# Performance work log

Hardware: AMD Instinct MI355X
Metric: run time of the kernel (lower is better)

Reference implementation:

```python
import jax, jax.numpy as jnp
import numpy as np


def _conv1x1(x, w, b=None):
    # x: [B,C,H,W], w: [O,C]
    y = jnp.einsum('bchw,oc->bohw', x, w)
    if b is not None:
        y = y + b[None, :, None, None]
    return y


def _conv3x3_dilated(x, w, b, dil):
    p = dil  # padding == dilation keeps spatial size for 3x3 kernels
    y = jax.lax.conv_general_dilated(
        x, w, window_strides=(1, 1), padding=((p, p), (p, p)),
        rhs_dilation=(dil, dil), dimension_numbers=('NCHW', 'OIHW', 'NCHW'))
    return y + b[None, :, None, None]


def _upsample2x_align_corners(x):
    # bilinear, align_corners=True, scale factor 2
    B, C, H, W = x.shape
    oh, ow = 2 * H, 2 * W
    ys = jnp.linspace(0.0, H - 1.0, oh)
    xs = jnp.linspace(0.0, W - 1.0, ow)
    y0 = jnp.floor(ys).astype(jnp.int32)
    x0 = jnp.floor(xs).astype(jnp.int32)
    y1 = jnp.minimum(y0 + 1, H - 1)
    x1 = jnp.minimum(x0 + 1, W - 1)
    wy = (ys - y0)[None, None, :, None]
    wx = (xs - x0)[None, None, None, :]
    gt = x[:, :, y0, :]
    gb = x[:, :, y1, :]
    top = gt[:, :, :, x0] * (1 - wx) + gt[:, :, :, x1] * wx
    bot = gb[:, :, :, x0] * (1 - wx) + gb[:, :, :, x1] * wx
    return top * (1 - wy) + bot * wy


def _gr(ftr, ck_w, ck_b, avg_w, max_w, gcn_w):
    # GR module: attention-diagonal graph conv with degree normalization
    B, C, H, W = ftr.shape
    HW = H * W
    # ChannelAttention_diag -> diagonal entries cw: [B, M]
    avg = ftr.mean(axis=(2, 3))
    mx = ftr.max(axis=(2, 3))
    cw = jax.nn.sigmoid(jax.nn.relu(avg @ avg_w.T) + jax.nn.relu(mx @ max_w.T))  # [B,M]
    k = jax.nn.relu(_conv1x1(ftr, ck_w, ck_b)).reshape(B, -1, HW)  # [B,M,HW]
    q = jnp.swapaxes(k, 1, 2)  # [B,HW,M]
    # A = sigmoid(q @ diag(cw) @ k); degree d = rowsum(A)^(-1/2)
    A = jax.nn.sigmoid(jnp.einsum('bim,bm,bmj->bij', q, cw, k))  # [B,HW,HW]
    d = A.sum(axis=2) ** -0.5  # [B,HW]
    P = d[:, :, None] * q  # D^{-1/2} @ q, [B,HW,M]
    X = jnp.swapaxes(ftr.reshape(B, C, HW), 1, 2)  # [B,HW,C]
    PtX = jnp.einsum('bjm,bjc->bmc', P, X)  # [B,M,C]
    LX = X - jnp.einsum('bim,bmc->bic', P, cw[:, :, None] * PtX)
    Y = X + LX @ gcn_w  # GCN (no bias)
    return jnp.swapaxes(Y, 1, 2).reshape(B, C, H, W)


def setup_inputs() -> dict:
    key = jax.random.key(0)
    ks = jax.random.split(key, 20)
    B, C = 64, 1024
    Cq = C // 4  # 256
    Mi = Cq // 2  # 128, ChannelAttention inter channels
    s = 0.02
    inp = {
        'x_cur': jax.random.normal(ks[0], (B, C, 16, 16), jnp.float32),
        'x_lat': jax.random.normal(ks[1], (B, C, 8, 8), jnp.float32),
        'conv_w': jax.random.normal(ks[2], (Cq, C), jnp.float32) * s,
        'conv_b': jax.random.normal(ks[3], (Cq,), jnp.float32) * s,
        'conv1_w': jax.random.normal(ks[4], (C, Cq), jnp.float32) * s,
        'conv1_b': jax.random.normal(ks[5], (C,), jnp.float32) * s,
        'conv3_w': jax.random.normal(ks[6], (C, 3 * Cq), jnp.float32) * s,
        'conv3_b': jax.random.normal(ks[7], (C,), jnp.float32) * s,
        'rate0_w': jax.random.normal(ks[8], (Cq, C, 3, 3), jnp.float32) * s,
        'rate0_b': jax.random.normal(ks[9], (Cq,), jnp.float32) * s,
        'rate1_w': jax.random.normal(ks[10], (Cq, C, 3, 3), jnp.float32) * s,
        'rate1_b': jax.random.normal(ks[11], (Cq,), jnp.float32) * s,
        'rate2_w': jax.random.normal(ks[12], (Cq, C, 3, 3), jnp.float32) * s,
        'rate2_b': jax.random.normal(ks[13], (Cq,), jnp.float32) * s,
        'gr_ck_w': jax.random.normal(ks[14], (Mi, Cq), jnp.float32) * s,
        'gr_ck_b': jax.random.normal(ks[15], (Mi,), jnp.float32) * s,
        'gr_avg_w': jax.random.normal(ks[16], (Mi, Cq), jnp.float32) * s,
        'gr_max_w': jax.random.normal(ks[17], (Mi, Cq), jnp.float32) * s,
        'gr_gcn_w': jax.random.normal(ks[18], (Cq, Cq), jnp.float32) * s,
        'pre': 1,
    }
    return inp


def reference(x_cur, x_lat, conv_w, conv_b, conv1_w, conv1_b, conv3_w, conv3_b,
              rate0_w, rate0_b, rate1_w, rate1_b, rate2_w, rate2_b,
              gr_ck_w, gr_ck_b, gr_avg_w, gr_max_w, gr_gcn_w, pre):
    # pre == 1 path of Graph_aspp.forward
    gr_args = (gr_ck_w, gr_ck_b, gr_avg_w, gr_max_w, gr_gcn_w)
    x_sum = x_cur * _upsample2x_align_corners(x_lat) + x_cur
    f1 = _conv3x3_dilated(x_sum, rate0_w, rate0_b, 1) + _conv1x1(x_sum, conv_w, conv_b)
    x1 = _gr(f1, *gr_args)
    feature = _conv1x1(f1, conv1_w, conv1_b) + x_sum
    f2 = _conv3x3_dilated(feature, rate1_w, rate1_b, 2) + _conv1x1(feature, conv_w, conv_b)
    x2 = _gr(f2, *gr_args)
    feature = _conv1x1(f2, conv1_w, conv1_b) + x_sum
    f3 = _conv3x3_dilated(feature, rate2_w, rate2_b, 4) + _conv1x1(feature, conv_w, conv_b)
    x3 = _gr(f3, *gr_args)
    cat = jnp.concatenate((x1, x2, x3), axis=1)
    return _conv1x1(cat, conv3_w, conv3_b)
```

## Files before the change

kernel.cpp:

```cpp
#include <hip/hip_runtime.h>

typedef unsigned short ushort_t;
typedef unsigned int uint32;
typedef __attribute__((ext_vector_type(8))) unsigned short ushort8;
typedef __attribute__((ext_vector_type(8))) __bf16 bf16x8;
typedef __attribute__((ext_vector_type(4))) float f32x4;

__device__ __forceinline__ ushort_t f2b(float f) {
    union { float f; uint32 u; } v; v.f = f;
    uint32 r = v.u + 0x7fffu + ((v.u >> 16) & 1u);
    return (ushort_t)(r >> 16);
}
__device__ __forceinline__ float b2f(ushort_t b) {
    union { uint32 u; float f; } v; v.u = ((uint32)b) << 16;
    return v.f;
}
__device__ __forceinline__ float sigm(float x) { return 1.f / (1.f + __expf(-x)); }

__device__ __forceinline__ void gload_lds16(const void* g, void* l) {
    __builtin_amdgcn_global_load_lds(
        (__attribute__((address_space(1))) void*)g,
        (__attribute__((address_space(3))) void*)l, 16, 0, 0);
}

constexpr int EPI_RELU  = 1;
constexpr int EPI_FQ    = 2;
constexpr int EPI_SIG   = 3;
constexpr int EPI_XG    = 4;
constexpr int EPI_NEGCW = 5;
constexpr int EPI_Y     = 6;
constexpr int EPI_OUTT  = 7;

struct GemmP {
    const ushort_t* A; const ushort_t* B;
    const ushort_t* A2; const ushort_t* B2;
    long long aBatch, bBatch, a2Batch, b2Batch;
    int lda, ldb, lda2, ldb2;
    int Ksub, kSplit, dil;
    const float* bias;
    const ushort_t* res; long long resBatch; int ldres;
    ushort_t* obf; long long oBatch; int ldo;
    ushort_t* obf2;
    float* of32;
    const float* cw;
    const float* rscale;
    float* dsum;
    const ushort_t* zpage;
};

__device__ __forceinline__ void big_body(ushort_t* aT, ushort_t* bT,
                                         const GemmP& p, int bx, int by, int z) {
    const int tid = threadIdx.x;
    const int m0 = bx * 128, n0 = by * 128;
    const int lane = tid & 63, wid = tid >> 6;
    const int l15 = lane & 15, l16 = lane >> 4;
    const int wr = wid >> 1, wc = wid & 1;
    const int lrow = lane >> 3;
    const int sgran = (lane & 7) ^ lrow;

    int ayy[4], axx[4];
    const ushort_t* aBase[4];
    const ushort_t* bBase[4];
#pragma unroll
    for (int i = 0; i < 4; ++i) {
        int row = wid * 32 + i * 8 + lrow;
        int m = m0 + row;
        int bb = m >> 8;
        ayy[i] = (m >> 4) & 15; axx[i] = m & 15;
        aBase[i] = p.A + (long long)bb * 262144 + sgran * 8;
        bBase[i] = p.B + (long long)(n0 + row) * p.ldb + sgran * 8;
    }

    f32x4 acc[4][4];
#pragma unroll
    for (int i = 0; i < 4; ++i)
#pragma unroll
        for (int j = 0; j < 4; ++j) acc[i][j] = (f32x4){0.f, 0.f, 0.f, 0.f};

    const int gk0 = z * p.kSplit;
    const int ntap = p.Ksub >> 10;
    for (int ti = 0; ti < ntap; ++ti) {
        const int tap = (gk0 >> 10) + ti;
        int dy = 0, dx = 0;
        if (tap < 9) { int ky = tap / 3; dy = (ky - 1) * p.dil; dx = (tap - ky * 3 - 1) * p.dil; }
        const ushort_t* gaA[4];
        const ushort_t* gaB[4];
#pragma unroll
        for (int i = 0; i < 4; ++i) {
            int iy = ayy[i] + dy, ix = axx[i] + dx;
            bool ok = ((unsigned)iy < 16u) && ((unsigned)ix < 16u);
            gaA[i] = ok ? (aBase[i] + (((iy << 4) + ix) << 10)) : (p.zpage + sgran * 8);
            gaB[i] = bBase[i] + (tap << 10);
        }
        for (int kk = 0; kk < 16; ++kk) {
            const int kin = kk << 6;
#pragma unroll
            for (int i = 0; i < 4; ++i)
                gload_lds16(gaA[i] + kin, &aT[(wid * 32 + i * 8) * 64]);
#pragma unroll
            for (int i = 0; i < 4; ++i)
                gload_lds16(gaB[i] + kin, &bT[(wid * 32 + i * 8) * 64]);
            asm volatile("s_waitcnt vmcnt(0)" ::: "memory");
            __syncthreads();
#pragma unroll
            for (int ks = 0; ks < 2; ++ks) {
                bf16x8 af[4], bfr[4];
#pragma unroll
                for (int mi = 0; mi < 4; ++mi) {
                    int rr = wr * 64 + mi * 16 + l15;
                    int cc = (ks * 32 + l16 * 8) ^ ((rr & 7) << 3);
                    af[mi] = __builtin_bit_cast(bf16x8, *(const ushort8*)&aT[rr * 64 + cc]);
                }
#pragma unroll
                for (int ni = 0; ni < 4; ++ni) {
                    int rr = wc * 64 + ni * 16 + l15;
                    int cc = (ks * 32 + l16 * 8) ^ ((rr & 7) << 3);
                    bfr[ni] = __builtin_bit_cast(bf16x8, *(const ushort8*)&bT[rr * 64 + cc]);
                }
#pragma unroll
                for (int mi = 0; mi < 4; ++mi)
#pragma unroll
                    for (int ni = 0; ni < 4; ++ni)
                        acc[mi][ni] = __builtin_amdgcn_mfma_f32_16x16x32_bf16(af[mi], bfr[ni], acc[mi][ni], 0, 0, 0);
            }
            __syncthreads();
        }
    }
#pragma unroll
    for (int mi = 0; mi < 4; ++mi)
#pragma unroll
        for (int ni = 0; ni < 4; ++ni) {
            int gcol = n0 + wc * 64 + ni * 16 + l15;
            int growb = m0 + wr * 64 + mi * 16 + l16 * 4;
#pragma unroll
            for (int r = 0; r < 4; ++r)
                p.obf[(long long)z * p.oBatch + (long long)(growb + r) * 256 + gcol] =
                    f2b(acc[mi][ni][r]);
        }
}

template<int BM, int BN, int AMODE, int EPI>
__device__ __forceinline__ void gemm_body(ushort_t* aT, ushort_t* bT,
                                          const GemmP& p, int bx, int by, int z) {
    constexpr int APASS = BM / 32, BPASS = BN / 32;
    constexpr int MFRAG = BM / 32, NFRAG = BN / 32;
    const int tid = threadIdx.x;
    const int m0 = bx * BM, n0 = by * BN;
    const int lane = tid & 63, wid = tid >> 6;
    const int l15 = lane & 15, l16 = lane >> 4;
    const int wr = wid >> 1, wc = wid & 1;
    const int srow = tid >> 3, scol = (tid & 7) * 8;
    const int swcol = scol ^ ((srow & 7) << 3);

    const ushort_t* aptr[APASS];
    const ushort_t* bptr[BPASS];
    const ushort_t* aptr2[APASS];
    const ushort_t* bptr2[BPASS];
    float rsA[APASS];
#pragma unroll
    for (int pi = 0; pi < APASS; ++pi)
        aptr[pi] = p.A + (long long)z * p.aBatch +
                   (long long)(m0 + pi * 32 + srow) * p.lda + scol;
#pragma unroll
    for (int pi = 0; pi < BPASS; ++pi)
        bptr[pi] = p.B + (long long)z * p.bBatch +
                   (long long)(n0 + pi * 32 + srow) * p.ldb + scol;
    if constexpr (AMODE == 2) {
#pragma unroll
        for (int pi = 0; pi < APASS; ++pi) {
            aptr2[pi] = p.A2 + (long long)z * p.a2Batch +
                        (long long)(m0 + pi * 32 + srow) * p.lda2 + scol;
            rsA[pi] = p.rscale[z * 256 + m0 + pi * 32 + srow];
        }
#pragma unroll
        for (int pi = 0; pi < BPASS; ++pi)
            bptr2[pi] = p.B2 + (long long)z * p.b2Batch +
                        (long long)(n0 + pi * 32 + srow) * p.ldb2 + scol;
    }

    f32x4 acc[MFRAG][NFRAG];
#pragma unroll
    for (int i = 0; i < MFRAG; ++i)
#pragma unroll
        for (int j = 0; j < NFRAG; ++j) acc[i][j] = (f32x4){0.f, 0.f, 0.f, 0.f};

    ushort8 ar[APASS], br[BPASS];
    auto ldg = [&](int gk) {
        if (AMODE == 2 && gk >= 256) {
            int g2 = gk - 256;
#pragma unroll
            for (int pi = 0; pi < APASS; ++pi) {
                ushort8 t8 = *(const ushort8*)(aptr2[pi] + g2);
#pragma unroll
                for (int k = 0; k < 8; ++k) t8[k] = f2b(b2f(t8[k]) * rsA[pi]);
                ar[pi] = t8;
            }
#pragma unroll
            for (int pi = 0; pi < BPASS; ++pi) br[pi] = *(const ushort8*)(bptr2[pi] + g2);
        } else if constexpr (AMODE == 3) {
#pragma unroll
            for (int pi = 0; pi < APASS; ++pi) {
                ushort8 t8 = *(const ushort8*)(aptr[pi] + gk);
#pragma unroll
                for (int k = 0; k < 8; ++k)
                    t8[k] = f2b(b2f(t8[k]) * p.cw[(z << 7) + gk + scol + k]);
                ar[pi] = t8;
            }
#pragma unroll
            for (int pi = 0; pi < BPASS; ++pi) br[pi] = *(const ushort8*)(bptr[pi] + gk);
        } else {
#pragma unroll
            for (int pi = 0; pi < APASS; ++pi) ar[pi] = *(const ushort8*)(aptr[pi] + gk);
#pragma unroll
            for (int pi = 0; pi < BPASS; ++pi) br[pi] = *(const ushort8*)(bptr[pi] + gk);
        }
    };

    const int gk0 = z * p.kSplit;
    ldg(gk0);
    const int iters = p.Ksub >> 6;
    for (int it = 0; it < iters; ++it) {
#pragma unroll
        for (int pi = 0; pi < APASS; ++pi)
            *(ushort8*)&aT[(pi * 32 + srow) * 64 + swcol] = ar[pi];
#pragma unroll
        for (int pi = 0; pi < BPASS; ++pi)
            *(ushort8*)&bT[(pi * 32 + srow) * 64 + swcol] = br[pi];
        __syncthreads();
        if (it + 1 < iters) ldg(gk0 + (it + 1) * 64);
#pragma unroll
        for (int ks = 0; ks < 2; ++ks) {
            bf16x8 af[MFRAG], bfr[NFRAG];
#pragma unroll
            for (int mi = 0; mi < MFRAG; ++mi) {
                int rr = wr * (BM / 2) + mi * 16 + l15;
                int cc = (ks * 32 + l16 * 8) ^ ((rr & 7) << 3);
                af[mi] = __builtin_bit_cast(bf16x8, *(const ushort8*)&aT[rr * 64 + cc]);
            }
#pragma unroll
            for (int ni = 0; ni < NFRAG; ++ni) {
                int rr = wc * (BN / 2) + ni * 16 + l15;
                int cc = (ks * 32 + l16 * 8) ^ ((rr & 7) << 3);
                bfr[ni] = __builtin_bit_cast(bf16x8, *(const ushort8*)&bT[rr * 64 + cc]);
            }
#pragma unroll
            for (int mi = 0; mi < MFRAG; ++mi)
#pragma unroll
                for (int ni = 0; ni < NFRAG; ++ni)
                    acc[mi][ni] = __builtin_amdgcn_mfma_f32_16x16x32_bf16(af[mi], bfr[ni], acc[mi][ni], 0, 0, 0);
        }
        __syncthreads();
    }

#pragma unroll
    for (int mi = 0; mi < MFRAG; ++mi) {
        if constexpr (EPI == EPI_SIG) {
#pragma unroll
            for (int r = 0; r < 4; ++r) {
                float sv = 0.f;
#pragma unroll
                for (int ni = 0; ni < NFRAG; ++ni) sv += sigm(acc[mi][ni][r]);
                sv += __shfl_xor(sv, 1); sv += __shfl_xor(sv, 2);
                sv += __shfl_xor(sv, 4); sv += __shfl_xor(sv, 8);
                if (l15 == 0) {
                    int grow = m0 + wr * (BM / 2) + mi * 16 + l16 * 4 + r;
                    int q8 = by * 2 + wc;
                    p.dsum[q8 * 16384 + z * 256 + grow] = sv;
                }
            }
        } else {
#pragma unroll
            for (int ni = 0; ni < NFRAG; ++ni) {
                int gcol = n0 + wc * (BN / 2) + ni * 16 + l15;
                int growb = m0 + wr * (BM / 2) + mi * 16 + l16 * 4;
#pragma unroll
                for (int r = 0; r < 4; ++r) {
                    int grow = growb + r;
                    float v = acc[mi][ni][r];
                    if constexpr (EPI == EPI_RELU) {
                        v += p.bias[gcol]; v = fmaxf(v, 0.f);
                        p.obf[(long long)grow * p.ldo + gcol] = f2b(v);
                    } else if constexpr (EPI == EPI_FQ) {
                        v += p.bias[gcol];
                        if (gcol < 1024) {
                            v += b2f(p.res[(long long)grow * 1024 + gcol]);
                            p.obf[(long long)grow * 1024 + gcol] = f2b(v);
                        } else {
                            v = fmaxf(v, 0.f);
                            p.obf2[(long long)grow * 128 + (gcol - 1024)] = f2b(v);
                        }
                    } else if constexpr (EPI == EPI_XG) {
                        p.obf[(long long)z * p.oBatch + (long long)grow * p.ldo + gcol] = f2b(v);
                    } else if constexpr (EPI == EPI_NEGCW) {
                        v *= -p.cw[z * 128 + gcol];
                        p.obf[(long long)z * p.oBatch + (long long)grow * p.ldo + gcol] = f2b(v);
                    } else if constexpr (EPI == EPI_Y) {
                        v = b2f(p.res[(long long)z * p.resBatch + (long long)grow * p.ldres + gcol]) + v;
                        p.obf[(long long)z * p.oBatch + (long long)grow * p.ldo + gcol] = f2b(v);
                    } else if constexpr (EPI == EPI_OUTT) {
                        v += p.bias[grow];
                        int bb = gcol >> 8, px = gcol & 255;
                        p.of32[((long long)bb * 1024 + grow) * 256 + px] = v;
                    }
                }
            }
        }
    }
}

template<int BM, int BN, int AMODE, int EPI>
__global__ __launch_bounds__(256) void gemm_k(GemmP p) {
    __shared__ __align__(16) ushort_t aT[BM * 64];
    __shared__ __align__(16) ushort_t bT[BN * 64];
    gemm_body<BM, BN, AMODE, EPI>(aT, bT, p, blockIdx.x, blockIdx.y, blockIdx.z);
}

__device__ __forceinline__ void pool_body(void* lds, int b, const ushort_t* f,
                                          const float* aw, const float* mw,
                                          float* cw) {
    float* sa = (float*)lds;
    float* sm = sa + 256;
    int t = threadIdx.x;
    float s = 0.f, m = -3.4e38f;
    const ushort_t* base = f + (long long)b * 65536 + t;
    for (int px = 0; px < 256; ++px) { float v = b2f(base[px * 256]); s += v; m = fmaxf(m, v); }
    sa[t] = s * (1.f / 256.f);
    sm[t] = m;
    __syncthreads();
    if (t < 128) {
        float s1 = 0.f, s2 = 0.f;
        const float* a = aw + t * 256; const float* w = mw + t * 256;
        for (int c = 0; c < 256; ++c) { s1 += sa[c] * a[c]; s2 += sm[c] * w[c]; }
        s1 = fmaxf(s1, 0.f); s2 = fmaxf(s2, 0.f);
        cw[b * 128 + t] = sigm(s1 + s2);
    }
}

__global__ __launch_bounds__(256) void k_big_sig_y(GemmP pb, GemmP ps, GemmP px,
                                                   GemmP py) {
    __shared__ __align__(16) ushort_t lds[2 * 128 * 64];
    int z = blockIdx.z;
    if (z < 5) { big_body(lds, lds + 8192, pb, blockIdx.x, blockIdx.y, z); return; }
    if (z < 13) {
        int flat = (z - 5) * 256 + blockIdx.y * 128 + blockIdx.x;
        int bx = flat & 3, by = (flat >> 2) & 3, bz = flat >> 4;
        if (bz < 64) gemm_body<64, 64, 3, EPI_SIG>(lds, lds + 4096, ps, bx, by, bz);
        else         gemm_body<64, 64, 0, EPI_XG>(lds, lds + 4096, px, bx, by, bz - 64);
        return;
    }
    int flat = (z - 13) * 256 + blockIdx.y * 128 + blockIdx.x;
    gemm_body<64, 64, 2, EPI_Y>(lds, lds + 4096, py, flat & 3, (flat >> 2) & 3, flat >> 4);
}

__global__ __launch_bounds__(256) void k_fqpool_htn(GemmP pf, GemmP ph,
                                                    const float* aw, const float* mw,
                                                    float* cw) {
    __shared__ __align__(16) ushort_t lds[2 * 128 * 64];
    int y = blockIdx.y;
    if (y < 9) { gemm_body<128, 128, 0, EPI_FQ>(lds, lds + 8192, pf, blockIdx.x, y, 0); return; }
    if (y == 9) { if (blockIdx.x < 64) pool_body(lds, blockIdx.x, pf.A, aw, mw, cw); return; }
    int flat = (y - 10) * 128 + blockIdx.x;
    gemm_body<64, 64, 0, EPI_NEGCW>(lds, lds + 4096, ph, flat & 3, (flat >> 2) & 1, flat >> 3);
}

__global__ __launch_bounds__(256) void k_qpool_htn(GemmP pq, GemmP ph,
                                                   const float* aw, const float* mw,
                                                   float* cw) {
    __shared__ __align__(16) ushort_t lds[2 * 64 * 64];
    int y = blockIdx.y;
    if (y < 2) { gemm_body<64, 64, 0, EPI_RELU>(lds, lds + 4096, pq, blockIdx.x, y, 0); return; }
    if (y == 2) { if (blockIdx.x < 64) pool_body(lds, blockIdx.x, pq.A, aw, mw, cw); return; }
    int flat = (y - 3) * 256 + blockIdx.x;
    gemm_body<64, 64, 0, EPI_NEGCW>(lds, lds + 4096, ph, flat & 3, (flat >> 2) & 1, flat >> 3);
}

__global__ __launch_bounds__(256) void k_sigxg_y(GemmP ps, GemmP px, GemmP py) {
    __shared__ __align__(16) ushort_t aT[64 * 64];
    __shared__ __align__(16) ushort_t bT[64 * 64];
    int z = blockIdx.z;
    if (z < 64)       gemm_body<64, 64, 3, EPI_SIG>(aT, bT, ps, blockIdx.x, blockIdx.y, z);
    else if (z < 128) gemm_body<64, 64, 0, EPI_XG>(aT, bT, px, blockIdx.x, blockIdx.y, z - 64);
    else              gemm_body<64, 64, 2, EPI_Y>(aT, bT, py, blockIdx.x, blockIdx.y, z - 128);
}


__global__ void k_combine(const ushort_t* __restrict__ t, const float* __restrict__ fbias_s,
                          ushort_t* __restrict__ f) {
    int idx = blockIdx.x * 256 + threadIdx.x;
    const long long N = 16384ll * 256;
    ushort8 a0 = *(const ushort8*)(t + (long long)idx * 8);
    ushort8 a1 = *(const ushort8*)(t + N + (long long)idx * 8);
    ushort8 a2 = *(const ushort8*)(t + 2 * N + (long long)idx * 8);
    ushort8 a3 = *(const ushort8*)(t + 3 * N + (long long)idx * 8);
    ushort8 a4 = *(const ushort8*)(t + 4 * N + (long long)idx * 8);
    int cb = (idx * 8) & 255;
    ushort8 o;
#pragma unroll
    for (int k = 0; k < 8; ++k)
        o[k] = f2b(b2f(a0[k]) + b2f(a1[k]) + b2f(a2[k]) + b2f(a3[k]) + b2f(a4[k]) + fbias_s[cb + k]);
    *(ushort8*)&f[(long long)idx * 8] = o;
}

__global__ void k_upsum(const float* __restrict__ xc, const float* __restrict__ xl,
                        ushort_t* __restrict__ xs) {
    __shared__ float lat[64 * 64];
    __shared__ ushort_t tile[64 * 258];
    int b = blockIdx.x, c0 = blockIdx.y * 64;
    int t = threadIdx.x;
    for (int i = t; i < 4096; i += 256)
        lat[i] = xl[((long long)(b * 1024 + c0 + (i >> 6))) * 64 + (i & 63)];
    __syncthreads();
    int y = t >> 4, x = t & 15;
    float fy = y * (7.f / 15.f); int y0 = (int)fy; float wy = fy - y0; int y1 = y0 + 1 > 7 ? 7 : y0 + 1;
    float fx = x * (7.f / 15.f); int x0 = (int)fx; float wx = fx - x0; int x1 = x0 + 1 > 7 ? 7 : x0 + 1;
    for (int cc = 0; cc < 64; ++cc) {
        float cur = xc[((long long)(b * 1024 + c0 + cc)) * 256 + t];
        const float* L = &lat[cc * 64];
        float tv = L[y0 * 8 + x0] * (1.f - wx) + L[y0 * 8 + x1] * wx;
        float bv = L[y1 * 8 + x0] * (1.f - wx) + L[y1 * 8 + x1] * wx;
        float up = tv + (bv - tv) * wy;
        tile[cc * 258 + t] = f2b(cur * (1.f + up));
    }
    __syncthreads();
    for (int i = t; i < 16384; i += 256) {
        int px = i >> 6, cc = i & 63;
        xs[((long long)(b * 256 + px)) * 1024 + c0 + cc] = tile[cc * 258 + px];
    }
}

__global__ void k_pscale(const ushort_t* __restrict__ q, const float* __restrict__ dsum8,
                         float* __restrict__ dscale, ushort_t* __restrict__ Pt) {
    __shared__ ushort_t t[128][130];
    __shared__ float dd[128];
    int jh = blockIdx.x, b = blockIdx.y;
    int j0 = jh * 128;
    int tid = threadIdx.x;
    if (tid < 128) {
        int pix = b * 256 + j0 + tid;
        float s = 0.f;
#pragma unroll
        for (int qs = 0; qs < 8; ++qs) s += dsum8[qs * 16384 + pix];
        float r = rsqrtf(s);
        dd[tid] = r;
        dscale[pix] = r;
    }
    __syncthreads();
    int jr = tid >> 7, m = tid & 127;
    for (int i = 0; i < 64; ++i) {
        int j = i * 2 + jr;
        long long qi = ((long long)(b * 256 + j0 + j)) * 128 + m;
        t[j][m] = f2b(dd[j] * b2f(q[qi]));
    }
    __syncthreads();
    for (int i = 0; i < 64; ++i) {
        int mm = i * 2 + jr;
        Pt[((long long)b << 15) + (mm << 8) + j0 + m] = t[m][mm];
    }
}

__global__ void k_packall(const float* r0, const float* r1, const float* r2,
                          const float* convw, const float* c1w, const float* c3w,
                          const float* ckw, const float* gcnw,
                          const float* rb0, const float* rb1, const float* rb2,
                          const float* cb, const float* c1b, const float* ckbias,
                          ushort_t* wbig3, ushort_t* wfq, ushort_t* w3b,
                          ushort_t* gcnT, float* fqbias, float* fbias,
                          ushort_t* zpage) {
    int blk = blockIdx.x, tid = threadIdx.x;
    if (blk < 768) {
        __shared__ float lw[10240];
        int s = blk >> 8, o = blk & 255;
        const float* rate = s == 0 ? r0 : (s == 1 ? r1 : r2);
        for (int i = tid; i < 9216; i += 256) lw[i] = rate[(long long)o * 9216 + i];
        for (int i = tid; i < 1024; i += 256) lw[9216 + i] = convw[(long long)o * 1024 + i];
        __syncthreads();
        ushort_t* dst = wbig3 + (long long)blk * 10240;
        for (int i = tid; i < 10240; i += 256) {
            int tap = i >> 10, ci = i & 1023;
            float v = (tap < 9) ? lw[ci * 9 + tap] : lw[9216 + ci];
            dst[i] = f2b(v);
        }
        return;
    }
    const int R1 = 262144;
    const int R2 = R1 + 32768;
    const int R3 = R2 + 786432;
    const int R4 = R3 + 65536;
    const int R5 = R4 + 1152;
    const int R6 = R5 + 768;
    const int R7 = R6 + 4096;
    int base = (blk - 768) * 2048 + tid * 8;
#pragma unroll
    for (int k = 0; k < 8; ++k) {
        int i = base + k;
        if (i >= R7) return;
        if (i < R1) wfq[i] = f2b(c1w[i]);
        else if (i < R2) wfq[i] = f2b(ckw[i - R1]);
        else if (i < R3) w3b[i - R2] = f2b(c3w[i - R2]);
        else if (i < R4) {
            int ii = i - R3; int c2 = ii >> 8, c1 = ii & 255;
            gcnT[ii] = f2b(gcnw[c1 * 256 + c2]);
        } else if (i < R5) {
            int ii = i - R4;
            fqbias[ii] = (ii < 1024) ? c1b[ii] : ckbias[ii - 1024];
        } else if (i < R6) {
            int ii = i - R5; int s = ii >> 8, t = ii & 255;
            const float* rb = s == 0 ? rb0 : (s == 1 ? rb1 : rb2);
            fbias[ii] = rb[t] + cb[t];
        } else {
            zpage[i - R6] = 0;
        }
    }
}

__global__ void k_sentinel(float* o, int n, float v) {
    int i = blockIdx.x * 256 + threadIdx.x; if (i < n) o[i] = v;
}

extern "C" void kernel_launch(void* const* d_in, const int* in_sizes, int n_in,
                              void* d_out, int out_size, void* d_ws, size_t ws_size,
                              hipStream_t stream) {
    const float* x_cur  = (const float*)d_in[0];
    const float* x_lat  = (const float*)d_in[1];
    const float* conv_w = (const float*)d_in[2];
    const float* conv_b = (const float*)d_in[3];
    const float* conv1_w = (const float*)d_in[4];
    const float* conv1_b = (const float*)d_in[5];
    const float* conv3_w = (const float*)d_in[6];
    const float* conv3_b = (const float*)d_in[7];
    const float* rate_w[3] = {(const float*)d_in[8], (const float*)d_in[10], (const float*)d_in[12]};
    const float* rate_b[3] = {(const float*)d_in[9], (const float*)d_in[11], (const float*)d_in[13]};
    const float* ck_w  = (const float*)d_in[14];
    const float* ck_b  = (const float*)d_in[15];
    const float* avg_w = (const float*)d_in[16];
    const float* max_w = (const float*)d_in[17];
    const float* gcn_w = (const float*)d_in[18];
    float* out = (float*)d_out;

    char* w = (char*)d_ws;
    auto take = [&](size_t bytes) { void* p = (void*)w; w += (bytes + 255) & ~(size_t)255; return p; };
    ushort_t* xsum   = (ushort_t*)take(16384ll * 1024 * 2);
    ushort_t* feat   = (ushort_t*)take(16384ll * 1024 * 2);
    ushort_t* fbufP[2];
    fbufP[0] = (ushort_t*)take(16384ll * 256 * 2);
    fbufP[1] = (ushort_t*)take(16384ll * 256 * 2);
    ushort_t* qbufP[2];
    qbufP[0] = (ushort_t*)take(16384ll * 128 * 2);
    qbufP[1] = (ushort_t*)take(16384ll * 128 * 2);
    ushort_t* xgt    = (ushort_t*)take(64ll * 256 * 256 * 2);
    ushort_t* Pt     = (ushort_t*)take(64ll * 128 * 256 * 2);
    ushort_t* Htn    = (ushort_t*)take(64ll * 256 * 128 * 2);
    ushort_t* wbig3  = (ushort_t*)take(3ll * 256 * 10240 * 2);
    ushort_t* wfq    = (ushort_t*)take(1152ll * 256 * 2);
    ushort_t* w3b    = (ushort_t*)take(1024ll * 768 * 2);
    ushort_t* gcnT   = (ushort_t*)take(256ll * 256 * 2);
    ushort_t* zpage  = (ushort_t*)take(8192);
    float*    fqbias = (float*)take(1152 * 4);
    float*    fbias  = (float*)take(3 * 256 * 4);
    float*    cwbP[2];
    cwbP[0] = (float*)take(64 * 128 * 4);
    cwbP[1] = (float*)take(64 * 128 * 4);
    float*    dscale = (float*)take(64 * 256 * 4);
    float*    dsum8  = (float*)take(8ll * 64 * 256 * 4);
    ushort_t* catb   = (ushort_t*)take(16384ll * 768 * 2);
    ushort_t* ftmp   = (ushort_t*)take(5ll * 16384 * 256 * 2);
    size_t need = (size_t)(w - (char*)d_ws);

    if (need > ws_size) {
        float v = 1.0e6f + (float)(ws_size >> 20);
        k_sentinel<<<(out_size + 255) / 256, 256, 0, stream>>>(out, out_size, v);
        return;
    }

    auto PBIG = [&](int s) {
        GemmP p{};
        p.A = (s == 0) ? xsum : feat;
        p.B = wbig3 + (long long)s * 256 * 10240; p.ldb = 10240;
        p.Ksub = 2048; p.kSplit = 2048; p.dil = 1 << s;
        p.obf = ftmp; p.oBatch = 16384ll * 256;
        p.zpage = zpage;
        return p;
    };
    auto PSIG = [&](int s) {
        GemmP p{};
        p.A = qbufP[s & 1]; p.aBatch = 32768; p.lda = 128;
        p.B = qbufP[s & 1]; p.bBatch = 32768; p.ldb = 128;
        p.Ksub = 128; p.dsum = dsum8; p.cw = cwbP[s & 1];
        return p;
    };
    auto PXG = [&](int s) {
        GemmP p{};
        p.A = gcnT; p.aBatch = 0;            p.lda = 256;
        p.B = fbufP[s & 1]; p.bBatch = 65536; p.ldb = 256;
        p.Ksub = 256;
        p.obf = xgt; p.oBatch = 65536; p.ldo = 256;
        return p;
    };
    auto PHTN = [&](int s) {
        GemmP p{};
        p.A = xgt; p.aBatch = 65536; p.lda = 256;
        p.B = Pt;  p.bBatch = 32768; p.ldb = 256;
        p.Ksub = 256; p.cw = cwbP[s & 1];
        p.obf = Htn; p.oBatch = 32768; p.ldo = 128;
        return p;
    };
    auto PY = [&](int s) {
        GemmP p{};
        p.A = fbufP[s & 1]; p.aBatch = 65536; p.lda = 256;
        p.B = gcnT; p.bBatch = 0;             p.ldb = 256;
        p.A2 = qbufP[s & 1]; p.a2Batch = 32768; p.lda2 = 128; p.rscale = dscale;
        p.B2 = Htn;          p.b2Batch = 32768; p.ldb2 = 128;
        p.Ksub = 384;
        p.res = fbufP[s & 1]; p.resBatch = 65536; p.ldres = 256;
        p.obf = catb + s * 256; p.oBatch = 256ll * 768; p.ldo = 768;
        return p;
    };
    auto PFQ = [&](int s) {
        GemmP p{};
        p.A = fbufP[s & 1]; p.lda = 256; p.B = wfq; p.ldb = 256;
        p.Ksub = 256; p.bias = fqbias;
        p.res = xsum;
        p.obf = feat; p.obf2 = qbufP[s & 1];
        return p;
    };
    GemmP pz{};

    k_packall<<<768 + 563, 256, 0, stream>>>(
        rate_w[0], rate_w[1], rate_w[2], conv_w, conv1_w, conv3_w, ck_w, gcn_w,
        rate_b[0], rate_b[1], rate_b[2], conv_b, conv1_b, ck_b,
        wbig3, wfq, w3b, gcnT, fqbias, fbias, zpage);
    k_upsum<<<dim3(64, 16), 256, 0, stream>>>(x_cur, x_lat, xsum);

    k_big_sig_y<<<dim3(128, 2, 5), 256, 0, stream>>>(PBIG(0), pz, pz, pz);
    k_combine<<<2048, 256, 0, stream>>>(ftmp, fbias + 0 * 256, fbufP[0]);
    k_fqpool_htn<<<dim3(128, 10), 256, 0, stream>>>(PFQ(0), pz, avg_w, max_w, cwbP[0]);
    k_big_sig_y<<<dim3(128, 2, 13), 256, 0, stream>>>(PBIG(1), PSIG(0), PXG(0), pz);
    k_combine<<<2048, 256, 0, stream>>>(ftmp, fbias + 1 * 256, fbufP[1]);
    k_pscale<<<dim3(2, 64), 256, 0, stream>>>(qbufP[0], dsum8, dscale, Pt);
    k_fqpool_htn<<<dim3(128, 14), 256, 0, stream>>>(PFQ(1), PHTN(0), avg_w, max_w, cwbP[1]);
    k_big_sig_y<<<dim3(128, 2, 17), 256, 0, stream>>>(PBIG(2), PSIG(1), PXG(1), PY(0));
    k_combine<<<2048, 256, 0, stream>>>(ftmp, fbias + 2 * 256, fbufP[0]);
    k_pscale<<<dim3(2, 64), 256, 0, stream>>>(qbufP[1], dsum8, dscale, Pt);
    {
        GemmP pq{};
        pq.A = fbufP[0]; pq.lda = 256; pq.B = wfq + 1024 * 256; pq.ldb = 256;
        pq.Ksub = 256;
        pq.bias = ck_b; pq.obf = qbufP[0]; pq.ldo = 128;
        k_qpool_htn<<<dim3(256, 5), 256, 0, stream>>>(pq, PHTN(1), avg_w, max_w, cwbP[0]);
    }
    k_sigxg_y<<<dim3(4, 4, 192), 256, 0, stream>>>(PSIG(2), PXG(2), PY(1));
    k_pscale<<<dim3(2, 64), 256, 0, stream>>>(qbufP[0], dsum8, dscale, Pt);
    gemm_k<64, 64, 0, EPI_NEGCW><<<dim3(4, 2, 64), 256, 0, stream>>>(PHTN(2));
    gemm_k<64, 64, 2, EPI_Y><<<dim3(4, 4, 64), 256, 0, stream>>>(PY(2));
    {
        GemmP p{};
        p.A = w3b;  p.lda = 768;
        p.B = catb; p.ldb = 768;
        p.Ksub = 768; p.bias = conv3_b; p.of32 = out;
        gemm_k<64, 128, 0, EPI_OUTT><<<dim3(16, 128, 1), 256, 0, stream>>>(p);
    }
}
```

Before: 626.0 us.

## Fuse split-K combine into big GEMM via last-block atomic counter

```diff
diff --git a/kernel.cpp b/kernel.cpp
--- a/kernel.cpp
+++ b/kernel.cpp
@@ -46,6 +46,7 @@
     const float* rscale;
     float* dsum;
     const ushort_t* zpage;
+    uint32* cnt;
 };
 
 __device__ __forceinline__ void big_body(ushort_t* aT, ushort_t* bT,
@@ -137,6 +138,28 @@
                 p.obf[(long long)z * p.oBatch + (long long)(growb + r) * 256 + gcol] =
                     f2b(acc[mi][ni][r]);
         }
+    __threadfence();
+    int* flagp = (int*)aT;
+    if (tid == 0) flagp[0] = (atomicAdd(p.cnt + (bx * 2 + by), 1u) == 4u) ? 1 : 0;
+    __syncthreads();
+    if (!flagp[0]) return;
+    __threadfence();
+    const long long N = p.oBatch;
+    for (int i = tid; i < 2048; i += 256) {
+        int r = i >> 4, c8 = (i & 15) << 3;
+        long long off = (long long)(m0 + r) * 256 + n0 + c8;
+        ushort8 a0 = *(const ushort8*)(p.obf + off);
+        ushort8 a1 = *(const ushort8*)(p.obf + N + off);
+        ushort8 a2 = *(const ushort8*)(p.obf + 2 * N + off);
+        ushort8 a3 = *(const ushort8*)(p.obf + 3 * N + off);
+        ushort8 a4 = *(const ushort8*)(p.obf + 4 * N + off);
+        ushort8 o;
+#pragma unroll
+        for (int k = 0; k < 8; ++k)
+            o[k] = f2b(b2f(a0[k]) + b2f(a1[k]) + b2f(a2[k]) + b2f(a3[k]) + b2f(a4[k]) +
+                       p.bias[n0 + c8 + k]);
+        *(ushort8*)(p.obf2 + off) = o;
+    }
 }
 
 template<int BM, int BN, int AMODE, int EPI>
@@ -384,23 +407,6 @@
 }
 
 
-__global__ void k_combine(const ushort_t* __restrict__ t, const float* __restrict__ fbias_s,
-                          ushort_t* __restrict__ f) {
-    int idx = blockIdx.x * 256 + threadIdx.x;
-    const long long N = 16384ll * 256;
-    ushort8 a0 = *(const ushort8*)(t + (long long)idx * 8);
-    ushort8 a1 = *(const ushort8*)(t + N + (long long)idx * 8);
-    ushort8 a2 = *(const ushort8*)(t + 2 * N + (long long)idx * 8);
-    ushort8 a3 = *(const ushort8*)(t + 3 * N + (long long)idx * 8);
-    ushort8 a4 = *(const ushort8*)(t + 4 * N + (long long)idx * 8);
-    int cb = (idx * 8) & 255;
-    ushort8 o;
-#pragma unroll
-    for (int k = 0; k < 8; ++k)
-        o[k] = f2b(b2f(a0[k]) + b2f(a1[k]) + b2f(a2[k]) + b2f(a3[k]) + b2f(a4[k]) + fbias_s[cb + k]);
-    *(ushort8*)&f[(long long)idx * 8] = o;
-}
-
 __global__ void k_upsum(const float* __restrict__ xc, const float* __restrict__ xl,
                         ushort_t* __restrict__ xs) {
     __shared__ float lat[64 * 64];
@@ -465,7 +471,7 @@
                           const float* cb, const float* c1b, const float* ckbias,
                           ushort_t* wbig3, ushort_t* wfq, ushort_t* w3b,
                           ushort_t* gcnT, float* fqbias, float* fbias,
-                          ushort_t* zpage) {
+                          ushort_t* zpage, uint32* cnt3) {
     int blk = blockIdx.x, tid = threadIdx.x;
     if (blk < 768) {
         __shared__ float lw[10240];
@@ -489,11 +495,12 @@
     const int R5 = R4 + 1152;
     const int R6 = R5 + 768;
     const int R7 = R6 + 4096;
+    const int R8 = R7 + 768;
     int base = (blk - 768) * 2048 + tid * 8;
 #pragma unroll
     for (int k = 0; k < 8; ++k) {
         int i = base + k;
-        if (i >= R7) return;
+        if (i >= R8) return;
         if (i < R1) wfq[i] = f2b(c1w[i]);
         else if (i < R2) wfq[i] = f2b(ckw[i - R1]);
         else if (i < R3) w3b[i - R2] = f2b(c3w[i - R2]);
@@ -507,8 +514,10 @@
             int ii = i - R5; int s = ii >> 8, t = ii & 255;
             const float* rb = s == 0 ? rb0 : (s == 1 ? rb1 : rb2);
             fbias[ii] = rb[t] + cb[t];
+        } else if (i < R7) {
+            zpage[i - R6] = 0;
         } else {
-            zpage[i - R6] = 0;
+            cnt3[i - R7] = 0;
         }
     }
 }
@@ -541,9 +550,10 @@
     auto take = [&](size_t bytes) { void* p = (void*)w; w += (bytes + 255) & ~(size_t)255; return p; };
     ushort_t* xsum   = (ushort_t*)take(16384ll * 1024 * 2);
     ushort_t* feat   = (ushort_t*)take(16384ll * 1024 * 2);
-    ushort_t* fbufP[2];
-    fbufP[0] = (ushort_t*)take(16384ll * 256 * 2);
-    fbufP[1] = (ushort_t*)take(16384ll * 256 * 2);
+    ushort_t* fbufA[3];
+    fbufA[0] = (ushort_t*)take(16384ll * 256 * 2);
+    fbufA[1] = (ushort_t*)take(16384ll * 256 * 2);
+    fbufA[2] = (ushort_t*)take(16384ll * 256 * 2);
     ushort_t* qbufP[2];
     qbufP[0] = (ushort_t*)take(16384ll * 128 * 2);
     qbufP[1] = (ushort_t*)take(16384ll * 128 * 2);
@@ -557,6 +567,7 @@
     ushort_t* zpage  = (ushort_t*)take(8192);
     float*    fqbias = (float*)take(1152 * 4);
     float*    fbias  = (float*)take(3 * 256 * 4);
+    uint32*   cnt3   = (uint32*)take(768 * 4);
     float*    cwbP[2];
     cwbP[0] = (float*)take(64 * 128 * 4);
     cwbP[1] = (float*)take(64 * 128 * 4);
@@ -578,6 +589,9 @@
         p.B = wbig3 + (long long)s * 256 * 10240; p.ldb = 10240;
         p.Ksub = 2048; p.kSplit = 2048; p.dil = 1 << s;
         p.obf = ftmp; p.oBatch = 16384ll * 256;
+        p.obf2 = fbufA[s];
+        p.bias = fbias + s * 256;
+        p.cnt = cnt3 + s * 256;
         p.zpage = zpage;
         return p;
     };
@@ -590,8 +604,8 @@
     };
     auto PXG = [&](int s) {
         GemmP p{};
-        p.A = gcnT; p.aBatch = 0;            p.lda = 256;
-        p.B = fbufP[s & 1]; p.bBatch = 65536; p.ldb = 256;
+        p.A = gcnT; p.aBatch = 0;           p.lda = 256;
+        p.B = fbufA[s]; p.bBatch = 65536;   p.ldb = 256;
         p.Ksub = 256;
         p.obf = xgt; p.oBatch = 65536; p.ldo = 256;
         return p;
@@ -606,18 +620,18 @@
     };
     auto PY = [&](int s) {
         GemmP p{};
-        p.A = fbufP[s & 1]; p.aBatch = 65536; p.lda = 256;
-        p.B = gcnT; p.bBatch = 0;             p.ldb = 256;
+        p.A = fbufA[s]; p.aBatch = 65536; p.lda = 256;
+        p.B = gcnT; p.bBatch = 0;         p.ldb = 256;
         p.A2 = qbufP[s & 1]; p.a2Batch = 32768; p.lda2 = 128; p.rscale = dscale;
         p.B2 = Htn;          p.b2Batch = 32768; p.ldb2 = 128;
         p.Ksub = 384;
-        p.res = fbufP[s & 1]; p.resBatch = 65536; p.ldres = 256;
+        p.res = fbufA[s]; p.resBatch = 65536; p.ldres = 256;
         p.obf = catb + s * 256; p.oBatch = 256ll * 768; p.ldo = 768;
         return p;
     };
     auto PFQ = [&](int s) {
         GemmP p{};
-        p.A = fbufP[s & 1]; p.lda = 256; p.B = wfq; p.ldb = 256;
+        p.A = fbufA[s]; p.lda = 256; p.B = wfq; p.ldb = 256;
         p.Ksub = 256; p.bias = fqbias;
         p.res = xsum;
         p.obf = feat; p.obf2 = qbufP[s & 1];
@@ -625,25 +639,22 @@
     };
     GemmP pz{};
 
-    k_packall<<<768 + 563, 256, 0, stream>>>(
+    k_packall<<<768 + 564, 256, 0, stream>>>(
         rate_w[0], rate_w[1], rate_w[2], conv_w, conv1_w, conv3_w, ck_w, gcn_w,
         rate_b[0], rate_b[1], rate_b[2], conv_b, conv1_b, ck_b,
-        wbig3, wfq, w3b, gcnT, fqbias, fbias, zpage);
+        wbig3, wfq, w3b, gcnT, fqbias, fbias, zpage, cnt3);
     k_upsum<<<dim3(64, 16), 256, 0, stream>>>(x_cur, x_lat, xsum);
 
     k_big_sig_y<<<dim3(128, 2, 5), 256, 0, stream>>>(PBIG(0), pz, pz, pz);
-    k_combine<<<2048, 256, 0, stream>>>(ftmp, fbias + 0 * 256, fbufP[0]);
     k_fqpool_htn<<<dim3(128, 10), 256, 0, stream>>>(PFQ(0), pz, avg_w, max_w, cwbP[0]);
     k_big_sig_y<<<dim3(128, 2, 13), 256, 0, stream>>>(PBIG(1), PSIG(0), PXG(0), pz);
-    k_combine<<<2048, 256, 0, stream>>>(ftmp, fbias + 1 * 256, fbufP[1]);
     k_pscale<<<dim3(2, 64), 256, 0, stream>>>(qbufP[0], dsum8, dscale, Pt);
     k_fqpool_htn<<<dim3(128, 14), 256, 0, stream>>>(PFQ(1), PHTN(0), avg_w, max_w, cwbP[1]);
     k_big_sig_y<<<dim3(128, 2, 17), 256, 0, stream>>>(PBIG(2), PSIG(1), PXG(1), PY(0));
-    k_combine<<<2048, 256, 0, stream>>>(ftmp, fbias + 2 * 256, fbufP[0]);
     k_pscale<<<dim3(2, 64), 256, 0, stream>>>(qbufP[1], dsum8, dscale, Pt);
     {
         GemmP pq{};
-        pq.A = fbufP[0]; pq.lda = 256; pq.B = wfq + 1024 * 256; pq.ldb = 256;
+        pq.A = fbufA[2]; pq.lda = 256; pq.B = wfq + 1024 * 256; pq.ldb = 256;
         pq.Ksub = 256;
         pq.bias = ck_b; pq.obf = qbufP[0]; pq.ldo = 128;
         k_qpool_htn<<<dim3(256, 5), 256, 0, stream>>>(pq, PHTN(1), avg_w, max_w, cwbP[0]);
```

Measured after the change: 1.280 ms. 104% more time.
